# Kernel optimization log

Measured on AMD Instinct MI355X. Metric: run time of the kernel, lower is better.

Reference implementation:

```python
import jax, jax.numpy as jnp
import numpy as np
import math

D_MODEL = 1024
N_HEADS = 16
HEAD_DIM = D_MODEL // N_HEADS
TEMP = 0.1          # sinkhorn temperature
SINK_ITERS = 10     # update_permutation uses n_iterations=10
EPS = 1e-10


def setup_inputs() -> dict:
    key = jax.random.key(0)
    ks = jax.random.split(key, 16)
    b, n, d = 2, 2048, D_MODEL
    x_data = jax.random.normal(ks[0], (b, n, d), dtype=jnp.float32)
    certainty = jax.random.uniform(ks[1], (b, n), dtype=jnp.float32)
    permutation = jnp.stack([jax.random.permutation(jax.random.fold_in(ks[2], i), n)
                             for i in range(b)]).astype(jnp.int64)
    def lin(k):
        kw, kb = jax.random.split(k)
        W = jax.random.normal(kw, (d, d), dtype=jnp.float32) * 0.02
        bvec = jax.random.normal(kb, (d,), dtype=jnp.float32) * 0.02
        return W, bvec
    Wq, bq = lin(ks[3]); Wk, bk = lin(ks[4]); Wv, bv = lin(ks[5]); Wo, bo = lin(ks[6])
    perm_bias_scale = jnp.ones((1, N_HEADS, 1, 1), dtype=jnp.float32)
    certainty_temp = jnp.ones((1,), dtype=jnp.float32) * 2.0
    return {"x_data": x_data, "certainty": certainty, "permutation": permutation,
            "Wq": Wq, "bq": bq, "Wk": Wk, "bk": bk, "Wv": Wv, "bv": bv,
            "Wo": Wo, "bo": bo, "perm_bias_scale": perm_bias_scale,
            "certainty_temp": certainty_temp}


def reference(x_data, certainty, permutation, Wq, bq, Wk, bk, Wv, bv, Wo, bo,
              perm_bias_scale, certainty_temp):
    b, n, d = x_data.shape
    scale = math.sqrt(HEAD_DIM)

    def proj(W, bias):  # nn.Linear: x @ W.T + b, then split heads -> (b,H,n,hd)
        y = jnp.einsum('bnd,ed->bne', x_data, W) + bias
        return y.reshape(b, n, N_HEADS, HEAD_DIM).transpose(0, 2, 1, 3)

    Q, K, V = proj(Wq, bq), proj(Wk, bk), proj(Wv, bv)

    scores = jnp.einsum('bhnk,bhmk->bhnm', Q, K) / scale  # (b,H,n,n)
    # permutation-distance bias: B[i,j] = -|sigma(i)-sigma(j)| * |scale_h|
    pf = permutation.astype(jnp.float32)
    dist = jnp.abs(pf[:, :, None] - pf[:, None, :])       # (b,n,n)
    scores = scores - dist[:, None, :, :] * jnp.abs(perm_bias_scale)

    attention = jax.nn.softmax(scores, axis=-1)           # dropout is identity (eval)
    out = jnp.einsum('bhnm,bhmd->bhnd', attention, V)
    out = out.transpose(0, 2, 1, 3).reshape(b, n, d)
    output = jnp.einsum('bnd,ed->bne', out, Wo) + bo

    # certainty update from attention entropy
    ent = -(attention * jnp.log(attention + EPS)).sum(-1).mean(1)  # (b,n)
    cert_upd = jax.nn.sigmoid(certainty_temp * (math.log(n) - ent))
    new_certainty = jnp.maximum(certainty, cert_upd)

    # permutation update via Sinkhorn on log mean attention
    avg_attn = attention.mean(axis=1)
    P = jnp.exp(jnp.log(avg_attn + EPS) / TEMP)
    def body(_, P):
        P = P / (P.sum(-1, keepdims=True) + EPS)
        P = P / (P.sum(-2, keepdims=True) + EPS)
        return P
    P = jax.lax.fori_loop(0, SINK_ITERS, body, P)
    idx = jnp.argmax(P, axis=-1)                          # (b,n)
    new_permutation = jnp.take_along_axis(permutation, idx, axis=1)

    return output, new_certainty, new_permutation
```

## Files before the change

kernel.cpp:

```cpp
#include <hip/hip_runtime.h>
#include <cstdint>

#define NTOK 2048
#define DMODEL 1024
#define NHEADS 16
#define HD 64
#define BATCH 2
#define EPSF 1e-10f
#define EPSD 1e-10

typedef __attribute__((ext_vector_type(8))) short bf16x8;
typedef __attribute__((ext_vector_type(8))) _Float16 f16x8;
typedef __attribute__((ext_vector_type(4))) float f32x4;

__device__ __forceinline__ float bf2f(unsigned short u){
  union { unsigned int i; float f; } c; c.i = ((unsigned int)u) << 16; return c.f;
}
__device__ __forceinline__ unsigned short f2bf(float f){
  union { float f; unsigned int u; } c; c.f = f;
  unsigned int u = c.u;
  unsigned int r = (u + 0x7FFFu + ((u >> 16) & 1u)) >> 16;
  return (unsigned short)r;
}
__device__ __forceinline__ unsigned short f2h(float f){
  union { _Float16 h; unsigned short u; } c; c.h = (_Float16)f; return c.u;
}
__device__ __forceinline__ float h2f(unsigned short u){
  union { unsigned short u; _Float16 h; } c; c.u = u; return (float)c.h;
}

__device__ __forceinline__ void async16(const unsigned short* g, unsigned short* lds_base){
  __builtin_amdgcn_global_load_lds((const __attribute__((address_space(1))) unsigned int*)g,
                                   (__attribute__((address_space(3))) unsigned int*)lds_base,
                                   16, 0, 0);
}

template<int CTRL>
__device__ __forceinline__ float dppmov(float x){
  union { float f; int i; } a, r;
  a.f = x;
  r.i = __builtin_amdgcn_update_dpp(0, a.i, CTRL, 0xF, 0xF, true);
  return r.f;
}
__device__ __forceinline__ float red16_max(float x){
  x = fmaxf(x, dppmov<0xB1>(x));
  x = fmaxf(x, dppmov<0x4E>(x));
  x = fmaxf(x, dppmov<0x124>(x));
  x = fmaxf(x, dppmov<0x128>(x));
  return x;
}
__device__ __forceinline__ float red16_sum(float x){
  x += dppmov<0xB1>(x);
  x += dppmov<0x4E>(x);
  x += dppmov<0x124>(x);
  x += dppmov<0x128>(x);
  return x;
}

template<int BM, int BN>
__device__ __forceinline__ void gemm_bt_core(
    const unsigned short* A, int lda,
    const unsigned short* B, int ldb,
    int K,
    f32x4 (&acc)[BM/32][BN/32],
    unsigned short* ldsA, unsigned short* ldsB)
{
  constexpr int TM = BM/32, TN = BN/32;
  const int tid  = threadIdx.x;
  const int lane = tid & 63;
  const int wave = tid >> 6;
  const int wm = wave >> 1, wn = wave & 1;
  const int fr = lane & 15;
  const int fk = (lane >> 4) << 3;
  const int sr = lane >> 2;
  const int sk = (lane & 3) << 3;

  for (int k0 = 0; k0 < K; k0 += 32){
    #pragma unroll
    for (int c = 0; c < BM/64; c++){
      int ch = c*4 + wave;
      async16(A + (long)(ch*16 + sr)*lda + (k0 + sk), ldsA + ch*512);
    }
    #pragma unroll
    for (int c = 0; c < BN/64; c++){
      int ch = c*4 + wave;
      async16(B + (long)(ch*16 + sr)*ldb + (k0 + sk), ldsB + ch*512);
    }
    __syncthreads();
    bf16x8 af[TM], bf[TN];
    #pragma unroll
    for (int i=0;i<TM;i++)
      af[i] = *(const bf16x8*)(ldsA + ((wm*TM*16) + i*16 + fr)*32 + fk);
    #pragma unroll
    for (int j=0;j<TN;j++)
      bf[j] = *(const bf16x8*)(ldsB + ((wn*TN*16) + j*16 + fr)*32 + fk);
    #pragma unroll
    for (int i=0;i<TM;i++)
      #pragma unroll
      for (int j=0;j<TN;j++)
        acc[i][j] = __builtin_amdgcn_mfma_f32_16x16x32_bf16(af[i], bf[j], acc[i][j], 0, 0, 0);
    __syncthreads();
  }
}

__device__ __forceinline__ double wred_sumd(double x){
  for(int o=32;o;o>>=1) x+=__shfl_xor(x,o); return x;
}


__global__ void init_kernel(double* __restrict__ uv){
  int idx = blockIdx.x*256 + threadIdx.x;
  if (idx < 8192) uv[idx] = 1.0;
}

__global__ void f2b_multi(const float* __restrict__ x,
    const float* __restrict__ wq, const float* __restrict__ wk,
    const float* __restrict__ wv, const float* __restrict__ wo,
    unsigned short* __restrict__ out)
{
  int i = blockIdx.x*256 + threadIdx.x;
  int base = i << 2;
  const float* src;
  if (base < 4194304) src = x + base;
  else {
    int d = base - 4194304;
    int r = d >> 20, off = d & 1048575;
    src = (r==0 ? wq : (r==1 ? wk : (r==2 ? wv : wo))) + off;
  }
  float4 v = *(const float4*)src;
  ushort4 o;
  o.x = f2bf(v.x); o.y = f2bf(v.y); o.z = f2bf(v.z); o.w = f2bf(v.w);
  *(ushort4*)(out + base) = o;
}

__global__ __launch_bounds__(256) void qkv_kernel(
    const unsigned short* __restrict__ xb,
    const unsigned short* __restrict__ Wqb, const float* __restrict__ bq,
    const unsigned short* __restrict__ Wkb, const float* __restrict__ bk,
    const unsigned short* __restrict__ Wvb, const float* __restrict__ bv,
    unsigned short* __restrict__ Qb, unsigned short* __restrict__ Kb,
    unsigned short* __restrict__ Vb)
{
  __shared__ unsigned short lds[(128+128)*32];
  int sel = blockIdx.y >> 3;
  int n0 = (blockIdx.y & 7) * 128;
  int m0 = blockIdx.x * 128;
  const unsigned short* W = sel==0 ? Wqb : (sel==1 ? Wkb : Wvb);
  const float* bias       = sel==0 ? bq  : (sel==1 ? bk  : bv);
  unsigned short* out     = sel==0 ? Qb  : (sel==1 ? Kb  : Vb);
  f32x4 acc[4][4];
  f32x4 z = {0.f,0.f,0.f,0.f};
  for (int i=0;i<4;i++) for(int j=0;j<4;j++) acc[i][j] = z;
  gemm_bt_core<128,128>(xb + (long)m0*DMODEL, DMODEL, W + (long)n0*DMODEL, DMODEL,
                        DMODEL, acc, lds, lds + 128*32);
  int lane = threadIdx.x & 63, wave = threadIdx.x >> 6;
  int wm = wave>>1, wn = wave&1;
  int cr = (lane>>4)<<2, cc = lane & 15;
  for (int i=0;i<4;i++) for(int j=0;j<4;j++) for(int r=0;r<4;r++){
    int row = m0 + wm*64 + i*16 + cr + r;
    int col = n0 + wn*64 + j*16 + cc;
    out[(long)row*DMODEL + col] = f2bf(acc[i][j][r] + bias[col]);
  }
}

__global__ void vtrans_kernel(const unsigned short* __restrict__ Vb,
                              unsigned short* __restrict__ Vt)
{
  __shared__ unsigned short t[32][33];
  int b = blockIdx.z, i0 = blockIdx.x*32, e0 = blockIdx.y*32;
  int tx = threadIdx.x, ty = threadIdx.y;
  for (int r=0;r<32;r+=8) t[ty+r][tx] = Vb[((long)b*NTOK + i0+ty+r)*DMODEL + e0+tx];
  __syncthreads();
  for (int r=0;r<32;r+=8)
    Vt[((long)b*DMODEL + e0+ty+r)*NTOK + i0+tx] = f2h(bf2f(t[tx][ty+r]));
}

__global__ __launch_bounds__(512,4) void attnA_kernel(
    const unsigned short* __restrict__ Qb, const unsigned short* __restrict__ Kb,
    const unsigned short* __restrict__ Vt, const int* __restrict__ perm,
    const float* __restrict__ psc,
    float* __restrict__ mpart, float* __restrict__ lpart, float* __restrict__ Tpart,
    unsigned short* __restrict__ Opart)
{
  __shared__ unsigned short Kt[2*128*32];
  __shared__ unsigned short Vtl[64*136];
  __shared__ unsigned short Pt[128*136];
  __shared__ unsigned short pbs[2048];

  const int tid  = threadIdx.x;
  const int lane = tid & 63;
  const int wave = tid >> 6;
  const int fr   = lane & 15;
  const int fkg  = lane >> 4;
  const int fk   = fkg << 3;
  const int cr   = fkg << 2;
  const int rw   = wave << 4;
  const int rt   = blockIdx.x >> 1;
  const int half = blockIdx.x & 1;
  const int m0   = rt * 128;
  const int h    = blockIdx.y;
  const int b    = blockIdx.z;

  const int fks = (fkg ^ ((fr >> 1) & 3)) << 3;

  for (int i = tid; i < 2048; i += 512) pbs[i] = (unsigned short)perm[b*NTOK + i];

  bf16x8 qf[2];
  #pragma unroll
  for (int kc=0;kc<2;kc++)
    qf[kc] = *(const bf16x8*)(Qb + ((long)(b*NTOK + m0 + rw + fr))*DMODEL + h*HD + kc*32 + fk);

  const float asc = fabsf(psc[h]);
  __syncthreads();

  float prow[4];
  #pragma unroll
  for (int r=0;r<4;r++) prow[r] = (float)pbs[m0 + rw + cr + r];

  float mrow[4], lrow[4], Trow[4];
  #pragma unroll
  for (int r=0;r<4;r++){ mrow[r] = -1e30f; lrow[r] = 0.f; Trow[r] = 0.f; }
  f32x4 oacc[4];
  {
    f32x4 z = {0.f,0.f,0.f,0.f};
    for (int jj=0;jj<4;jj++) oacc[jj]=z;
  }

  for (int j2=0;j2<8;j2++){
    int j = half*8 + j2;
    __syncthreads();
    #pragma unroll
    for (int c=0;c<2;c++){
      int q = c*8 + wave;
      int kc = q >> 3, rb = (q & 7) * 16;
      async16(Kb + ((long)(b*NTOK + j*128 + rb + (lane>>2)))*DMODEL + h*HD + kc*32
                 + ((((lane&3) ^ ((lane>>3)&3)))<<3),
              Kt + kc*4096 + rb*32);
    }
    {
      int c = tid>>3, sg = tid&7;
      const unsigned short* vg = Vt + ((long)(b*DMODEL + h*HD + c))*NTOK + j*128 + sg*16;
      unsigned short* vl = Vtl + c*136 + sg*16;
      *(uint4*)(vl)   = *(const uint4*)(vg);
      *(uint4*)(vl+8) = *(const uint4*)(vg+8);
    }
    __syncthreads();

    f32x4 sacc[8];
    {
      f32x4 z = {0.f,0.f,0.f,0.f};
      for (int jj=0;jj<8;jj++) sacc[jj]=z;
    }
    #pragma unroll
    for (int kc=0;kc<2;kc++){
      bf16x8 bfr[8];
      #pragma unroll
      for (int jj=0;jj<8;jj++)
        bfr[jj] = *(const bf16x8*)(Kt + kc*4096 + (jj*16+fr)*32 + fks);
      #pragma unroll
      for (int jj=0;jj<8;jj++)
        sacc[jj] = __builtin_amdgcn_mfma_f32_16x16x32_bf16(qf[kc], bfr[jj], sacc[jj],0,0,0);
    }

    float pcol[8];
    #pragma unroll
    for (int jj=0;jj<8;jj++) pcol[jj] = (float)pbs[j*128 + jj*16 + fr];

    #pragma unroll
    for (int r=0;r<4;r++){
      float sv[8];
      float tm = -1e30f;
      #pragma unroll
      for (int jj=0;jj<8;jj++){
        sv[jj] = sacc[jj][r]*0.125f - fabsf(prow[r]-pcol[jj])*asc;
        tm = fmaxf(tm, sv[jj]);
      }
      tm = red16_max(tm);
      float nm = fmaxf(mrow[r], tm);
      float alpha = __expf(mrow[r] - nm);
      float lres = lrow[r]*alpha;
      Trow[r] = Trow[r]*alpha + (mrow[r]-nm)*lres;
      #pragma unroll
      for (int jc=0;jc<4;jc++) oacc[jc][r] *= alpha;
      float ts=0.f, tT=0.f;
      int prowbase = (rw + cr + r)*136;
      #pragma unroll
      for (int jj=0;jj<8;jj++){
        float d = sv[jj]-nm;
        float ev = __expf(d);
        ts += ev; tT += ev*d;
        Pt[prowbase + jj*16 + fr] = f2h(ev);
      }
      ts = red16_sum(ts);
      tT = red16_sum(tT);
      lrow[r] = lres + ts;
      Trow[r] += tT;
      mrow[r] = nm;
    }
    __syncthreads();
    #pragma unroll
    for (int kp=0;kp<4;kp++){
      f16x8 paf, pbf[4];
      paf = *(const f16x8*)(Pt + (rw+fr)*136 + kp*32 + fk);
      #pragma unroll
      for (int jj=0;jj<4;jj++) pbf[jj] = *(const f16x8*)(Vtl + (jj*16+fr)*136 + kp*32 + fk);
      #pragma unroll
      for (int jj=0;jj<4;jj++)
        oacc[jj] = __builtin_amdgcn_mfma_f32_16x16x32_f16(paf, pbf[jj], oacc[jj],0,0,0);
    }
  }

  long pbase = ((long)(half*BATCH + b)*NHEADS + h)*NTOK;
  #pragma unroll
  for (int jj=0;jj<4;jj++)
    #pragma unroll
    for (int r=0;r<4;r++){
      int row = m0 + rw + cr + r;
      Opart[(pbase + row)*HD + jj*16 + fr] = f2bf(oacc[jj][r]);
    }
  if (fr == 0){
    #pragma unroll
    for (int r=0;r<4;r++){
      int row = m0 + rw + cr + r;
      mpart[pbase + row] = mrow[r];
      lpart[pbase + row] = lrow[r];
      Tpart[pbase + row] = Trow[r];
    }
  }
}

__global__ __launch_bounds__(256) void merge_kernel(
    const float* __restrict__ mpart, const float* __restrict__ lpart,
    const float* __restrict__ Tpart, const unsigned short* __restrict__ Opart,
    unsigned short* __restrict__ Ob, float* __restrict__ mbuf,
    float* __restrict__ ilbuf, float* __restrict__ entb)
{
  int tid = threadIdx.x;
  int row = blockIdx.x*4 + (tid>>6);
  int h = blockIdx.y;
  int b = blockIdx.z;
  int col = tid & 63;
  long o1 = ((long)(0*BATCH + b)*NHEADS + h)*NTOK + row;
  long o2 = ((long)(1*BATCH + b)*NHEADS + h)*NTOK + row;
  float m1 = mpart[o1], m2 = mpart[o2];
  float l1 = lpart[o1], l2 = lpart[o2];
  float m = fmaxf(m1, m2);
  float e1 = __expf(m1-m), e2 = __expf(m2-m);
  float l = l1*e1 + l2*e2;
  float il = 1.0f/l;
  float Ov = (bf2f(Opart[o1*HD + col])*e1 + bf2f(Opart[o2*HD + col])*e2)*il;
  Ob[((long)(b*NTOK + row))*DMODEL + h*HD + col] = f2bf(Ov);
  if (col == 0){
    float T = e1*(Tpart[o1] + (m1-m)*l1) + e2*(Tpart[o2] + (m2-m)*l2);
    long off = ((long)(b*NHEADS+h))*NTOK + row;
    mbuf[off] = m; ilbuf[off] = il;
    entb[off] = T*il - __logf(l);
  }
}

__global__ __launch_bounds__(512,4) void avgP_kernel(
    const unsigned short* __restrict__ Qb, const unsigned short* __restrict__ Kb,
    const int* __restrict__ perm, const float* __restrict__ psc,
    const float* __restrict__ mbuf, const float* __restrict__ ilbuf,
    float* __restrict__ avg, unsigned short* __restrict__ avgH,
    unsigned short* __restrict__ avgT)
{
  __shared__ unsigned short Kt[2][8192];
  __shared__ float sm[NHEADS*64];
  __shared__ float si[NHEADS*64];
  __shared__ float sasc[NHEADS];

  const int bid = blockIdx.x;
  const int xcd = bid & 7, idx = bid >> 3;
  const int b   = xcd >> 2;
  const int qy  = (xcd >> 1) & 1, qx = xcd & 1;
  const int ydim = qy*16 + (idx >> 3);
  const int xdim = qx*8  + (idx & 7);
  const int m0   = ydim * 64;
  const int colb = xdim * 128;

  const int tid  = threadIdx.x;
  const int lane = tid & 63;
  const int wave = tid >> 6;
  const int wr = wave >> 2, wc = wave & 3;
  const int rw = wr*32, cb = wc*32;
  const int fr = lane & 15;
  const int fk = (lane >> 4) << 3;
  const int cr = (lane >> 4) << 2;
  const int cc = lane & 15;
  const int sr = lane >> 2;
  const int sk = (lane & 3) << 3;

  const unsigned short* kgp[2];
  int ldsoff[2];
  #pragma unroll
  for (int q=0;q<2;q++){
    int cid = q*8 + wave;
    int kc = cid >> 3, ch = cid & 7;
    kgp[q] = Kb + ((long)(b*NTOK + colb + ch*16 + sr))*DMODEL + kc*32 + sk;
    ldsoff[q] = kc*4096 + ch*512;
  }

  for (int e = tid; e < NHEADS*64; e += 512){
    int h = e >> 6, r = e & 63;
    long off = ((long)(b*NHEADS + h))*NTOK + m0 + r;
    sm[e] = mbuf[off];
    si[e] = ilbuf[off];
  }
  if (tid < NHEADS) sasc[tid] = fabsf(psc[tid]);

  float prw[8];
  #pragma unroll
  for (int i=0;i<2;i++)
    #pragma unroll
    for (int r=0;r<4;r++)
      prw[i*4+r] = (float)perm[b*NTOK + m0 + rw + i*16 + cr + r];
  float pcl[2];
  #pragma unroll
  for (int j=0;j<2;j++)
    pcl[j] = (float)perm[b*NTOK + colb + cb + j*16 + cc];

  const unsigned short* qp[2];
  #pragma unroll
  for (int i=0;i<2;i++)
    qp[i] = Qb + ((long)(b*NTOK + m0 + rw + i*16 + fr))*DMODEL + fk;

  float aacc[2][2][4];
  #pragma unroll
  for (int i=0;i<2;i++) for (int j=0;j<2;j++) for (int r=0;r<4;r++) aacc[i][j][r]=0.f;

  #pragma unroll
  for (int q=0;q<2;q++) async16(kgp[q], &Kt[0][0] + ldsoff[q]);
  __syncthreads();

  unsigned short* curb = &Kt[0][0];
  unsigned short* nxtb = &Kt[1][0];

  #pragma unroll 2
  for (int h=0; h<NHEADS; h++){
    if (h < NHEADS-1){
      #pragma unroll
      for (int q=0;q<2;q++) async16(kgp[q] + (h+1)*HD, nxtb + ldsoff[q]);
    }
    bf16x8 qf[2][2];
    #pragma unroll
    for (int i=0;i<2;i++)
      #pragma unroll
      for (int kc=0;kc<2;kc++)
        qf[i][kc] = *(const bf16x8*)(qp[i] + h*HD + kc*32);

    f32x4 acc[2][2];
    {
      f32x4 z = {0.f,0.f,0.f,0.f};
      acc[0][0]=z; acc[0][1]=z; acc[1][0]=z; acc[1][1]=z;
    }
    #pragma unroll
    for (int kc=0;kc<2;kc++){
      bf16x8 bfr[2];
      #pragma unroll
      for (int j=0;j<2;j++)
        bfr[j] = *(const bf16x8*)(curb + kc*4096 + ((cb>>4) + j)*512 + fr*32 + fk);
      #pragma unroll
      for (int i=0;i<2;i++)
        #pragma unroll
        for (int j=0;j<2;j++)
          acc[i][j] = __builtin_amdgcn_mfma_f32_16x16x32_bf16(qf[i][kc], bfr[j], acc[i][j],0,0,0);
    }
    const float asc = sasc[h];
    #pragma unroll
    for (int i=0;i<2;i++)
      #pragma unroll
      for (int r=0;r<4;r++){
        int rl = rw + i*16 + cr + r;
        float mh = sm[h*64 + rl];
        float ih = si[h*64 + rl];
        #pragma unroll
        for (int j=0;j<2;j++){
          float sv = acc[i][j][r]*0.125f - fabsf(prw[i*4+r]-pcl[j])*asc;
          aacc[i][j][r] += __expf(sv - mh) * ih;
        }
      }
    __syncthreads();
    unsigned short* t = curb; curb = nxtb; nxtb = t;
  }

  unsigned short* T = &Kt[0][0];
  #pragma unroll
  for (int i=0;i<2;i++)
    #pragma unroll
    for (int j=0;j<2;j++)
      #pragma unroll
      for (int r=0;r<4;r++){
        float pw = __expf(__logf(aacc[i][j][r]*0.0625f + EPSF)*10.0f);
        int rl = rw + i*16 + cr + r;
        int cl = cb + j*16 + cc;
        long off = ((long)(b*NTOK + m0 + rl))*NTOK + colb + cl;
        avg[off] = pw;
        unsigned short hv = f2h(pw);
        avgH[off] = hv;
        T[cl*72 + rl] = hv;
      }
  __syncthreads();
  {
    int c = tid >> 2, sg = tid & 3;
    uint4* dst = (uint4*)(avgT + ((long)(b*NTOK + colb + c))*NTOK + m0 + sg*16);
    const unsigned short* src = T + c*72 + sg*16;
    dst[0] = *(const uint4*)(src);
    dst[1] = *(const uint4*)(src + 8);
  }
}

__global__ __launch_bounds__(256) void sink_phase_h(const unsigned short* __restrict__ M,
    const double* __restrict__ x, double* __restrict__ y)
{
  int b = blockIdx.y, tid = threadIdx.x;
  int wave = tid >> 6, lane = tid & 63;
  int i = blockIdx.x*4 + wave;
  const unsigned short* row = M + ((long)b*NTOK + i)*NTOK;
  const double* xb = x + b*NTOK;
  double s = 0.0;
  #pragma unroll
  for (int k=0;k<4;k++){
    int j = k*512 + lane*8;
    f16x8 mv = *(const f16x8*)(row + j);
    #pragma unroll
    for (int e=0;e<8;e++) s += (double)(float)mv[e] * xb[j+e];
  }
  s = wred_sumd(s);
  if (lane == 0){
    double yi = y[b*NTOK + i];
    y[b*NTOK + i] = yi / (yi*s + EPSD);
  }
}

__global__ __launch_bounds__(256) void argmax_kernel(const float* __restrict__ P,
    const double* __restrict__ v, const int* __restrict__ perm,
    float* __restrict__ dout_perm)
{
  int b = blockIdx.y, tid = threadIdx.x;
  int wave = tid >> 6, lane = tid & 63;
  int i = blockIdx.x*4 + wave;
  const float* row = P + ((long)b*NTOK + i)*NTOK;
  const double* vb = v + b*NTOK;
  double bv = -1.0; int bj = 0;
  #pragma unroll
  for (int k=0;k<4;k++){
    int j0 = k*512 + lane*8;
    float4 r0 = *(const float4*)(row + j0);
    float4 r1 = *(const float4*)(row + j0 + 4);
    float rv[8] = {r0.x,r0.y,r0.z,r0.w,r1.x,r1.y,r1.z,r1.w};
    #pragma unroll
    for (int e=0;e<8;e++){
      double val = (double)rv[e]*vb[j0+e];
      if (val>bv){ bv=val; bj=j0+e; }
    }
  }
  for (int o=32;o;o>>=1){
    double ov=__shfl_xor(bv,o); int oj=__shfl_xor(bj,o);
    if (ov>bv || (ov==bv && oj<bj)){bv=ov;bj=oj;}
  }
  if (lane == 0)
    dout_perm[b*NTOK + i] = (float)perm[b*NTOK + bj];
}

__global__ __launch_bounds__(256) void out_kernel(
    const unsigned short* __restrict__ Ob, const unsigned short* __restrict__ Wob,
    const float* __restrict__ bo, float* __restrict__ dout)
{
  __shared__ unsigned short lds[(128+128)*32];
  int m0 = blockIdx.x*128, n0 = blockIdx.y*128;
  f32x4 acc[4][4];
  f32x4 z = {0.f,0.f,0.f,0.f};
  for (int i=0;i<4;i++) for(int j=0;j<4;j++) acc[i][j] = z;
  gemm_bt_core<128,128>(Ob + (long)m0*DMODEL, DMODEL, Wob + (long)n0*DMODEL, DMODEL,
                        DMODEL, acc, lds, lds + 128*32);
  int lane = threadIdx.x & 63, wave = threadIdx.x >> 6;
  int wm = wave>>1, wn = wave&1;
  int cr = (lane>>4)<<2, cc = lane & 15;
  for (int i=0;i<4;i++) for(int j=0;j<4;j++) for(int r=0;r<4;r++){
    int row = m0 + wm*64 + i*16 + cr + r;
    int col = n0 + wn*64 + j*16 + cc;
    dout[(long)row*DMODEL + col] = acc[i][j][r] + bo[col];
  }
}

__global__ void cert_kernel(const float* __restrict__ cert,
    const float* __restrict__ ctemp, const float* __restrict__ entb,
    float* __restrict__ dout_cert)
{
  int idx = blockIdx.x*256+threadIdx.x;
  if (idx >= BATCH*NTOK) return;
  int b = idx >> 11, row = idx & 2047;
  float s = 0.f;
  #pragma unroll
  for (int h=0; h<NHEADS; h++) s += entb[((long)(b*NHEADS+h))*NTOK + row];
  float ent = -s * (1.0f/16.0f);
  float ct = ctemp[0];
  float arg = ct * (logf((float)NTOK) - ent);
  float upd = 1.0f/(1.0f+expf(-arg));
  dout_cert[idx] = fmaxf(cert[idx], upd);
}

extern "C" void kernel_launch(void* const* d_in, const int* in_sizes, int n_in,
                              void* d_out, int out_size, void* d_ws, size_t ws_size,
                              hipStream_t stream)
{
  const float* x    = (const float*)d_in[0];
  const float* cert = (const float*)d_in[1];
  const int*   perm = (const int*)d_in[2];
  const float* Wq   = (const float*)d_in[3];
  const float* bq   = (const float*)d_in[4];
  const float* Wk   = (const float*)d_in[5];
  const float* bk   = (const float*)d_in[6];
  const float* Wv   = (const float*)d_in[7];
  const float* bv   = (const float*)d_in[8];
  const float* Wo   = (const float*)d_in[9];
  const float* bo   = (const float*)d_in[10];
  const float* psc  = (const float*)d_in[11];
  const float* ctmp = (const float*)d_in[12];
  float* dout = (float*)d_out;

  double* u    = (double*)d_ws;
  double* v    = u + 4096;
  float* avg   = (float*)(v + 4096);
  float* mbuf  = avg   + 8388608;
  float* ilbuf = mbuf  + 65536;
  float* entb  = ilbuf + 65536;
  float* mpart = entb  + 65536;
  float* lpart = mpart + 131072;
  float* Tpart = lpart + 131072;
  unsigned short* Opart = (unsigned short*)(Tpart + 131072);
  unsigned short* xb  = Opart + 8388608;
  unsigned short* Wqb = xb  + 4194304;
  unsigned short* Wkb = Wqb + 1048576;
  unsigned short* Wvb = Wkb + 1048576;
  unsigned short* Wob = Wvb + 1048576;
  unsigned short* Qb  = Wob + 1048576;
  unsigned short* Kb  = Qb  + 4194304;
  unsigned short* Vb  = Kb  + 4194304;
  unsigned short* Vt  = Vb  + 4194304;
  unsigned short* Ob  = Vt  + 4194304;
  unsigned short* avgH = Opart;
  unsigned short* avgT = Vb;

  f2b_multi<<<dim3(8192),256,0,stream>>>(x, Wq, Wk, Wv, Wo, xb);
  init_kernel<<<dim3(32),256,0,stream>>>(u);

  qkv_kernel<<<dim3(32,24),256,0,stream>>>(xb, Wqb,bq, Wkb,bk, Wvb,bv, Qb,Kb,Vb);
  vtrans_kernel<<<dim3(64,32,2), dim3(32,8),0,stream>>>(Vb, Vt);

  attnA_kernel<<<dim3(32,NHEADS,2),512,0,stream>>>(Qb, Kb, Vt, perm, psc,
      mpart, lpart, Tpart, Opart);
  merge_kernel<<<dim3(512,NHEADS,2),256,0,stream>>>(mpart, lpart, Tpart, Opart,
      Ob, mbuf, ilbuf, entb);
  avgP_kernel<<<dim3(1024),512,0,stream>>>(Qb, Kb, perm, psc, mbuf, ilbuf,
      avg, avgH, avgT);

  for (int it=0; it<10; it++){
    sink_phase_h<<<dim3(512,2),256,0,stream>>>(avgH, v, u);
    sink_phase_h<<<dim3(512,2),256,0,stream>>>(avgT, u, v);
  }
  argmax_kernel<<<dim3(512,2),256,0,stream>>>(avg, v, perm, dout + 4194304 + 4096);

  out_kernel <<<dim3(32,8),256,0,stream>>>(Ob, Wob, bo, dout);
  cert_kernel<<<dim3(16), 256,0,stream>>>(cert, ctmp, entb, dout + 4194304);
}
```

Before: 478.0 us.

## Switch Sinkhorn scaling vectors to fp32 and fold softmax scale into Q

Converts the Sinkhorn row/column scaling vectors, the matrix-vector reductions and the argmax from double to float, and vectorizes the x loads in sink_phase_h as float4 with two partial sums. Also folds the 1/sqrt(head_dim) factor into the Q projection epilogue so the attention kernels skip a multiply per score. The goal is to avoid slow fp64 arithmetic and shuffles in the many Sinkhorn passes. The cost is lower precision in the scaling factors, where the P values are raised to the 10th power, so overflow or underflow could change argmax ties.

```diff
diff --git a/kernel.cpp b/kernel.cpp
--- a/kernel.cpp
+++ b/kernel.cpp
@@ -7,7 +7,6 @@
 #define HD 64
 #define BATCH 2
 #define EPSF 1e-10f
-#define EPSD 1e-10
 
 typedef __attribute__((ext_vector_type(8))) short bf16x8;
 typedef __attribute__((ext_vector_type(8))) _Float16 f16x8;
@@ -103,14 +102,14 @@
   }
 }
 
-__device__ __forceinline__ double wred_sumd(double x){
+__device__ __forceinline__ float wred_sumf(float x){
   for(int o=32;o;o>>=1) x+=__shfl_xor(x,o); return x;
 }
 
 
-__global__ void init_kernel(double* __restrict__ uv){
+__global__ void init_kernel(float* __restrict__ uv){
   int idx = blockIdx.x*256 + threadIdx.x;
-  if (idx < 8192) uv[idx] = 1.0;
+  if (idx < 8192) uv[idx] = 1.0f;
 }
 
 __global__ void f2b_multi(const float* __restrict__ x,
@@ -148,6 +147,7 @@
   const unsigned short* W = sel==0 ? Wqb : (sel==1 ? Wkb : Wvb);
   const float* bias       = sel==0 ? bq  : (sel==1 ? bk  : bv);
   unsigned short* out     = sel==0 ? Qb  : (sel==1 ? Kb  : Vb);
+  const float qs          = sel==0 ? 0.125f : 1.0f;
   f32x4 acc[4][4];
   f32x4 z = {0.f,0.f,0.f,0.f};
   for (int i=0;i<4;i++) for(int j=0;j<4;j++) acc[i][j] = z;
@@ -159,7 +159,7 @@
   for (int i=0;i<4;i++) for(int j=0;j<4;j++) for(int r=0;r<4;r++){
     int row = m0 + wm*64 + i*16 + cr + r;
     int col = n0 + wn*64 + j*16 + cc;
-    out[(long)row*DMODEL + col] = f2bf(acc[i][j][r] + bias[col]);
+    out[(long)row*DMODEL + col] = f2bf((acc[i][j][r] + bias[col])*qs);
   }
 }
 
@@ -272,7 +272,7 @@
       float tm = -1e30f;
       #pragma unroll
       for (int jj=0;jj<8;jj++){
-        sv[jj] = sacc[jj][r]*0.125f - fabsf(prow[r]-pcol[jj])*asc;
+        sv[jj] = sacc[jj][r] - fabsf(prow[r]-pcol[jj])*asc;
         tm = fmaxf(tm, sv[jj]);
       }
       tm = red16_max(tm);
@@ -476,7 +476,7 @@
         float ih = si[h*64 + rl];
         #pragma unroll
         for (int j=0;j<2;j++){
-          float sv = acc[i][j][r]*0.125f - fabsf(prw[i*4+r]-pcl[j])*asc;
+          float sv = acc[i][j][r] - fabsf(prw[i*4+r]-pcl[j])*asc;
           aacc[i][j][r] += __expf(sv - mh) * ih;
         }
       }
@@ -511,38 +511,40 @@
 }
 
 __global__ __launch_bounds__(256) void sink_phase_h(const unsigned short* __restrict__ M,
-    const double* __restrict__ x, double* __restrict__ y)
+    const float* __restrict__ x, float* __restrict__ y)
 {
   int b = blockIdx.y, tid = threadIdx.x;
   int wave = tid >> 6, lane = tid & 63;
   int i = blockIdx.x*4 + wave;
   const unsigned short* row = M + ((long)b*NTOK + i)*NTOK;
-  const double* xb = x + b*NTOK;
-  double s = 0.0;
+  const float* xb = x + b*NTOK;
+  float s0 = 0.f, s1 = 0.f;
   #pragma unroll
   for (int k=0;k<4;k++){
     int j = k*512 + lane*8;
     f16x8 mv = *(const f16x8*)(row + j);
-    #pragma unroll
-    for (int e=0;e<8;e++) s += (double)(float)mv[e] * xb[j+e];
-  }
-  s = wred_sumd(s);
+    float4 x0 = *(const float4*)(xb + j);
+    float4 x1 = *(const float4*)(xb + j + 4);
+    s0 += (float)mv[0]*x0.x + (float)mv[2]*x0.z + (float)mv[4]*x1.x + (float)mv[6]*x1.z;
+    s1 += (float)mv[1]*x0.y + (float)mv[3]*x0.w + (float)mv[5]*x1.y + (float)mv[7]*x1.w;
+  }
+  float s = wred_sumf(s0 + s1);
   if (lane == 0){
-    double yi = y[b*NTOK + i];
-    y[b*NTOK + i] = yi / (yi*s + EPSD);
+    float yi = y[b*NTOK + i];
+    y[b*NTOK + i] = yi / (yi*s + EPSF);
   }
 }
 
 __global__ __launch_bounds__(256) void argmax_kernel(const float* __restrict__ P,
-    const double* __restrict__ v, const int* __restrict__ perm,
+    const float* __restrict__ v, const int* __restrict__ perm,
     float* __restrict__ dout_perm)
 {
   int b = blockIdx.y, tid = threadIdx.x;
   int wave = tid >> 6, lane = tid & 63;
   int i = blockIdx.x*4 + wave;
   const float* row = P + ((long)b*NTOK + i)*NTOK;
-  const double* vb = v + b*NTOK;
-  double bv = -1.0; int bj = 0;
+  const float* vb = v + b*NTOK;
+  float bv = -1.0f; int bj = 0;
   #pragma unroll
   for (int k=0;k<4;k++){
     int j0 = k*512 + lane*8;
@@ -551,12 +553,12 @@
     float rv[8] = {r0.x,r0.y,r0.z,r0.w,r1.x,r1.y,r1.z,r1.w};
     #pragma unroll
     for (int e=0;e<8;e++){
-      double val = (double)rv[e]*vb[j0+e];
+      float val = rv[e]*vb[j0+e];
       if (val>bv){ bv=val; bj=j0+e; }
     }
   }
   for (int o=32;o;o>>=1){
-    double ov=__shfl_xor(bv,o); int oj=__shfl_xor(bj,o);
+    float ov=__shfl_xor(bv,o); int oj=__shfl_xor(bj,o);
     if (ov>bv || (ov==bv && oj<bj)){bv=ov;bj=oj;}
   }
   if (lane == 0)
@@ -620,9 +622,9 @@
   const float* ctmp = (const float*)d_in[12];
   float* dout = (float*)d_out;
 
-  double* u    = (double*)d_ws;
-  double* v    = u + 4096;
-  float* avg   = (float*)(v + 4096);
+  float* u     = (float*)d_ws;
+  float* v     = u + 4096;
+  float* avg   = v + 4096;
   float* mbuf  = avg   + 8388608;
   float* ilbuf = mbuf  + 65536;
   float* entb  = ilbuf + 65536;
```

After: 425.1 us. -11.1%, faster.
